# Optimization experiments

Measured on AMD Instinct MI355X. Metric: run time of the kernel, lower is better.

The kernel has to match this reference:

```python
import jax, jax.numpy as jnp
import numpy as np

K = 7            # spatial grid size (k x k bins, k^2 score-map channels)
H = W = 1024     # score map resolution


def setup_inputs() -> dict:
    key = jax.random.key(0)
    x = jax.random.normal(key, (K * K, H, W), dtype=jnp.float32)
    # ijhw fractional region: center (0.5, 0.5), height/width 0.6 -> fully in-bounds
    region = jnp.array([0.5, 0.5, 0.6, 0.6], dtype=jnp.float32)
    return {"x": x, "region": region}


def reference(x, region):
    """Position-sensitive ROI pooling (R-FCN, arXiv:1605.06409).

    x: (k^2, H, W) score map; channel c = i*k + j is read by bin (i, j).
    region: (4,) ijhw fractional (center-i, center-j, h, w).
    Returns scalar: mean over k^2 bins of the per-bin spatial mean.

    Instead of k^2 python-level variable-size slices + means (irregular access
    in the original), each bin's floor/ceil integer extent is expressed as a
    separable row/col 0-1 mask, and all bin sums are fused into one einsum.
    """
    k = K
    k2, xh, xw = x.shape
    i, j, h, w = region[0], region[1], region[2], region[3]

    # ijhw -> ijij corners of the full region
    i0, j0 = i - h / 2, j - w / 2
    i1, j1 = i + h / 2, j + w / 2

    # bin centers: interior k points of a (k+2)-point linspace across the region
    ic = jnp.linspace(i0, i1, k + 2)[1:-1]            # (k,)
    jc = jnp.linspace(j0, j1, k + 2)[1:-1]            # (k,)
    bh, bw = h / k, w / k                             # bin height / width

    # per-bin integer pixel extents: floor(start), ceil(end), scaled to H, W
    ri0 = jnp.floor((ic - bh / 2) * xh)               # (k,)
    ri1 = jnp.ceil((ic + bh / 2) * xh)
    rj0 = jnp.floor((jc - bw / 2) * xw)
    rj1 = jnp.ceil((jc + bw / 2) * xw)

    rows = jnp.arange(xh, dtype=x.dtype)
    cols = jnp.arange(xw, dtype=x.dtype)
    # separable membership masks: mi[i, r] = 1 if row r in bin-row i
    mi = ((rows[None, :] >= ri0[:, None]) & (rows[None, :] < ri1[:, None])).astype(x.dtype)  # (k, H)
    mj = ((cols[None, :] >= rj0[:, None]) & (cols[None, :] < rj1[:, None])).astype(x.dtype)  # (k, W)

    x4 = x.reshape(k, k, xh, xw)                      # channel c = i*k + j -> (i, j)
    sums = jnp.einsum('ijhw,ih,jw->ij', x4, mi, mj)   # (k, k) per-bin sums
    counts = mi.sum(-1)[:, None] * mj.sum(-1)[None, :]  # (k, k) per-bin pixel counts
    bin_scores = sums / counts                        # per-bin spatial mean
    return bin_scores.mean()                          # scalar region score
```

## Files before the change

### kernel.cpp

```cpp
#include <hip/hip_runtime.h>


#define KK 7
#define HH 1024
#define WW 1024

__global__ __launch_bounds__(256) void psroi_bin_kernel(
    const float* __restrict__ x,
    const float* __restrict__ region,
    float* __restrict__ ws)
{
#pragma clang fp contract(off)
    const int b  = blockIdx.x;
    const int bi = b / KK;
    const int bj = b - bi * KK;

    const float ci = region[0];
    const float cj = region[1];
    const float h  = region[2];
    const float w  = region[3];

    const float i0  = ci - h / 2.0f;
    const float i1f = ci + h / 2.0f;
    const float j0  = cj - w / 2.0f;
    const float j1f = cj + w / 2.0f;

    const float di = (i1f - i0) / (float)(KK + 1);
    const float dj = (j1f - j0) / (float)(KK + 1);

    const float ic = i0 + (float)(bi + 1) * di;
    const float jc = j0 + (float)(bj + 1) * dj;

    const float bh2 = (h / (float)KK) / 2.0f;
    const float bw2 = (w / (float)KK) / 2.0f;

    int r0 = (int)floorf((ic - bh2) * (float)HH);
    int r1 = (int)ceilf ((ic + bh2) * (float)HH);
    int c0 = (int)floorf((jc - bw2) * (float)WW);
    int c1 = (int)ceilf ((jc + bw2) * (float)WW);
    r0 = max(0, r0);  r1 = min(HH, r1);
    c0 = max(0, c0);  c1 = min(WW, c1);

    const int nr = max(0, r1 - r0);
    const int nc = max(0, c1 - c0);
    const int n  = nr * nc;

    const float* __restrict__ xc = x + (size_t)b * (size_t)(HH * WW);

    float acc = 0.0f;
    for (int idx = threadIdx.x; idx < n; idx += 256) {
        const int r = idx / nc;
        const int c = idx - r * nc;
        acc += xc[(size_t)(r0 + r) * WW + (size_t)(c0 + c)];
    }

    #pragma unroll
    for (int off = 32; off > 0; off >>= 1)
        acc += __shfl_down(acc, off, 64);

    __shared__ float wsum[4];
    const int lane = threadIdx.x & 63;
    const int wid  = threadIdx.x >> 6;
    if (lane == 0) wsum[wid] = acc;
    __syncthreads();

    if (threadIdx.x == 0) {
        const float s = (wsum[0] + wsum[1]) + (wsum[2] + wsum[3]);
        ws[b] = s / (float)n;
    }
}

__global__ __launch_bounds__(64) void psroi_final_kernel(
    const float* __restrict__ ws,
    float* __restrict__ out)
{
    const int t = threadIdx.x;
    float v = (t < KK * KK) ? ws[t] : 0.0f;
    #pragma unroll
    for (int off = 32; off > 0; off >>= 1)
        v += __shfl_down(v, off, 64);
    if (t == 0) out[0] = v / (float)(KK * KK);
}

extern "C" void kernel_launch(void* const* d_in, const int* in_sizes, int n_in,
                              void* d_out, int out_size, void* d_ws, size_t ws_size,
                              hipStream_t stream) {
    const float* x      = (const float*)d_in[0];
    const float* region = (const float*)d_in[1];
    float* out = (float*)d_out;
    float* ws  = (float*)d_ws;

    psroi_bin_kernel<<<KK * KK, 256, 0, stream>>>(x, region, ws);
    psroi_final_kernel<<<1, 64, 0, stream>>>(ws, out);
}
```

Measured before the change: 244.1 us.

## Split each bin across four blocks and iterate rows per wavefront

Each bin's reduction is now spread over four blocks (196 instead of 49), so more compute units share the memory-bound sum. The flat index loop with an integer divide per element is replaced by a row loop, where each wavefront reads contiguous columns of its rows. The final kernel recomputes the bin pixel counts and combines the four partial sums per bin. The cost is a larger workspace and a slightly different floating-point summation order.

```diff
diff --git a/kernel.cpp b/kernel.cpp
--- a/kernel.cpp
+++ b/kernel.cpp
@@ -5,16 +5,11 @@
 #define HH 1024
 #define WW 1024
 
-__global__ __launch_bounds__(256) void psroi_bin_kernel(
-    const float* __restrict__ x,
-    const float* __restrict__ region,
-    float* __restrict__ ws)
-{
+struct Ext { int r0, r1, c0, c1; };
+
+__device__ __forceinline__ Ext bin_extent(const float* __restrict__ region,
+                                          int bi, int bj) {
 #pragma clang fp contract(off)
-    const int b  = blockIdx.x;
-    const int bi = b / KK;
-    const int bj = b - bi * KK;
-
     const float ci = region[0];
     const float cj = region[1];
     const float h  = region[2];
@@ -34,24 +29,38 @@
     const float bh2 = (h / (float)KK) / 2.0f;
     const float bw2 = (w / (float)KK) / 2.0f;
 
-    int r0 = (int)floorf((ic - bh2) * (float)HH);
-    int r1 = (int)ceilf ((ic + bh2) * (float)HH);
-    int c0 = (int)floorf((jc - bw2) * (float)WW);
-    int c1 = (int)ceilf ((jc + bw2) * (float)WW);
-    r0 = max(0, r0);  r1 = min(HH, r1);
-    c0 = max(0, c0);  c1 = min(WW, c1);
+    Ext e;
+    e.r0 = max(0, (int)floorf((ic - bh2) * (float)HH));
+    e.r1 = min(HH, (int)ceilf ((ic + bh2) * (float)HH));
+    e.c0 = max(0, (int)floorf((jc - bw2) * (float)WW));
+    e.c1 = min(WW, (int)ceilf ((jc + bw2) * (float)WW));
+    return e;
+}
 
-    const int nr = max(0, r1 - r0);
-    const int nc = max(0, c1 - c0);
-    const int n  = nr * nc;
+__global__ __launch_bounds__(256) void psroi_partial_kernel(
+    const float* __restrict__ x,
+    const float* __restrict__ region,
+    float* __restrict__ ws)
+{
+    const int blk  = blockIdx.x;
+    const int b    = blk >> 2;
+    const int part = blk & 3;
+    const int bi   = b / KK;
+    const int bj   = b - bi * KK;
+
+    const Ext e  = bin_extent(region, bi, bj);
+    const int nc = e.c1 - e.c0;
 
     const float* __restrict__ xc = x + (size_t)b * (size_t)(HH * WW);
 
+    const int lane = threadIdx.x & 63;
+    const int wid  = threadIdx.x >> 6;
+
     float acc = 0.0f;
-    for (int idx = threadIdx.x; idx < n; idx += 256) {
-        const int r = idx / nc;
-        const int c = idx - r * nc;
-        acc += xc[(size_t)(r0 + r) * WW + (size_t)(c0 + c)];
+    for (int r = e.r0 + part + 4 * wid; r < e.r1; r += 16) {
+        const float* __restrict__ row = xc + (size_t)r * WW + e.c0;
+        for (int c = lane; c < nc; c += 64)
+            acc += row[c];
     }
 
     #pragma unroll
@@ -59,27 +68,32 @@
         acc += __shfl_down(acc, off, 64);
 
     __shared__ float wsum[4];
-    const int lane = threadIdx.x & 63;
-    const int wid  = threadIdx.x >> 6;
     if (lane == 0) wsum[wid] = acc;
     __syncthreads();
 
-    if (threadIdx.x == 0) {
-        const float s = (wsum[0] + wsum[1]) + (wsum[2] + wsum[3]);
-        ws[b] = s / (float)n;
-    }
+    if (threadIdx.x == 0)
+        ws[blk] = (wsum[0] + wsum[1]) + (wsum[2] + wsum[3]);
 }
 
 __global__ __launch_bounds__(64) void psroi_final_kernel(
+    const float* __restrict__ region,
     const float* __restrict__ ws,
     float* __restrict__ out)
 {
     const int t = threadIdx.x;
-    float v = (t < KK * KK) ? ws[t] : 0.0f;
+    float mean = 0.0f;
+    if (t < KK * KK) {
+        const int bi = t / KK;
+        const int bj = t - bi * KK;
+        const Ext e = bin_extent(region, bi, bj);
+        const int n = (e.r1 - e.r0) * (e.c1 - e.c0);
+        const float s = (ws[4 * t] + ws[4 * t + 1]) + (ws[4 * t + 2] + ws[4 * t + 3]);
+        mean = s / (float)n;
+    }
     #pragma unroll
     for (int off = 32; off > 0; off >>= 1)
-        v += __shfl_down(v, off, 64);
-    if (t == 0) out[0] = v / (float)(KK * KK);
+        mean += __shfl_down(mean, off, 64);
+    if (t == 0) out[0] = mean / (float)(KK * KK);
 }
 
 extern "C" void kernel_launch(void* const* d_in, const int* in_sizes, int n_in,
@@ -90,6 +104,6 @@
     float* out = (float*)d_out;
     float* ws  = (float*)d_ws;
 
-    psroi_bin_kernel<<<KK * KK, 256, 0, stream>>>(x, region, ws);
-    psroi_final_kernel<<<1, 64, 0, stream>>>(ws, out);
+    psroi_partial_kernel<<<KK * KK * 4, 256, 0, stream>>>(x, region, ws);
+    psroi_final_kernel<<<1, 64, 0, stream>>>(region, ws, out);
 }
```

Result: faster. 235.4 us (-3.5%).
